# Kernel tuning notes

Measured on AMD Instinct MI355X. Metric: run time of the kernel, lower is better.

Reference implementation:

```python
import jax, jax.numpy as jnp
import numpy as np

TEMP = 0.07
BASE_TEMP = 0.07
BANK = 8192
B = 512      # samples per view; features has 2*B rows
D = 128      # feature dim
N_CLASSES = 100


def _l2norm(x, axis=-1):
    return x / jnp.linalg.norm(x, axis=axis, keepdims=True)


def setup_inputs() -> dict:
    key = jax.random.key(0)
    k1, k2, k3, k4, k5 = jax.random.split(key, 5)
    # SupCon features are L2-normalized embeddings; two views stacked: [2B, 1, D]
    features = _l2norm(jax.random.normal(k1, (2 * B, 1, D), jnp.float32))
    label = jax.random.randint(k2, (B,), 0, N_CLASSES)
    # memory banks stored as [D, bank_size] (lightly MemoryBankModule layout)
    bank1 = _l2norm(jax.random.normal(k3, (D, BANK), jnp.float32), axis=0)
    bank2 = _l2norm(jax.random.normal(k4, (D, BANK), jnp.float32), axis=0)
    bank_labels = jax.random.randint(k5, (BANK,), 0, N_CLASSES)
    return {"features": features, "label": label, "bank1": bank1,
            "bank2": bank2, "bank_labels": bank_labels}


def _branch_loss(cf, pos_mask, neg_mask):
    # cf: [N, D] anchor==contrast features
    logits = jnp.matmul(cf, cf.T) / TEMP                       # [N, N]
    logits = logits - jax.lax.stop_gradient(logits.max(axis=1, keepdims=True))
    # denominator: sum of exp(logits) over NEGATIVES only (square(mask-1) mask)
    denom = jnp.log((jnp.exp(logits) * neg_mask).sum(axis=1, keepdims=True))
    log_prob = logits - denom                                  # [N, N]
    mean_log_prob_pos = (pos_mask * log_prob).sum(axis=1) / pos_mask.sum(axis=1)
    return -(TEMP / BASE_TEMP) * mean_log_prob_pos             # [N]


def reference(features, label, bank1, bank2, bank_labels):
    d = features.shape[-1]
    fr = features.reshape(-1, d)                # [2B, D]
    nb = fr.shape[0] // 2
    f1, f2 = fr[:nb], fr[nb:]                   # [B, D] each

    labels_all = jnp.concatenate([bank_labels.reshape(-1, 1),
                                  label.reshape(-1, 1)], axis=0)   # [N, 1]
    same = (labels_all == labels_all.T)                            # [N, N]
    mask = same.astype(fr.dtype)
    n = mask.shape[0]
    self_mask = 1.0 - jnp.eye(n, dtype=fr.dtype)
    pos_mask = mask * self_mask                 # positives excluding self
    neg_mask = jnp.square(mask - 1.0)           # 1 where labels differ

    cf1 = jnp.concatenate([bank2.T, f1], axis=0)   # [N, D]
    cf2 = jnp.concatenate([bank1.T, f2], axis=0)   # [N, D]

    class_loss = (_branch_loss(cf1, pos_mask, neg_mask)
                  + _branch_loss(cf2, pos_mask, neg_mask)) / 2.0
    loss = class_loss.mean()
    return (loss, loss, loss)
```

## Files before the change

kernel.cpp:

```cpp
#include <hip/hip_runtime.h>
#include <math.h>

#define NTOT 8704
#define BANKN 8192
#define NB 512
#define DIM 128
#define INVT (1.0f / 0.07f)
#define C2L 20.6099131801f
#define NCHUNK 17
#define TPC 8
#define BN 64

using short8 = __attribute__((ext_vector_type(8))) short;
using ushort8 = __attribute__((ext_vector_type(8))) unsigned short;
using f32x4 = __attribute__((ext_vector_type(4))) float;

static __device__ __forceinline__ ushort f2bf(float f) {
  union { float f; unsigned u; } v;
  v.f = f;
  unsigned r = v.u + 0x7fffu + ((v.u >> 16) & 1u);
  return (ushort)(r >> 16);
}

static __device__ __forceinline__ float fast_exp2(float x) {
#if __has_builtin(__builtin_amdgcn_exp2f)
  return __builtin_amdgcn_exp2f(x);
#else
  return exp2f(x);
#endif
}

__global__ void prep1_kernel(const int* __restrict__ bank_labels,
                             const int* __restrict__ label,
                             int* __restrict__ cnt,
                             float* __restrict__ zp) {
  const int i = blockIdx.x * 256 + threadIdx.x;
  reinterpret_cast<float4*>(zp)[i] = make_float4(0.f, 0.f, 0.f, 0.f);
  const int v = (i < BANKN) ? bank_labels[i] : label[i - BANKN];
  atomicAdd(&cnt[v], 1);
}

__global__ void prep2_kernel(const int* __restrict__ cnt,
                             int* __restrict__ st, int* __restrict__ cur) {
  __shared__ int sc[128];
  const int tid = threadIdx.x;
  int mine = (tid < 100) ? cnt[tid] : 0;
  sc[tid] = mine;
  __syncthreads();
#pragma unroll
  for (int off = 1; off < 128; off <<= 1) {
    int add = (tid >= off) ? sc[tid - off] : 0;
    __syncthreads();
    sc[tid] += add;
    __syncthreads();
  }
  if (tid < 100) {
    const int ex = sc[tid] - mine;
    st[tid] = ex;
    cur[tid] = ex;
    if (tid == 99) st[100] = sc[99];
  }
}

__global__ void prep3_kernel(const int* __restrict__ bank_labels,
                             const int* __restrict__ label,
                             const int* __restrict__ st, int* __restrict__ cur,
                             int* __restrict__ inv, int* __restrict__ lo,
                             int* __restrict__ hi) {
  const int i = blockIdx.x * 256 + threadIdx.x;
  const int v = (i < BANKN) ? bank_labels[i] : label[i - BANKN];
  const int p = atomicAdd(&cur[v], 1);
  inv[i] = p;
  lo[p] = st[v];
  hi[p] = st[v + 1];
}

__global__ void pack_kernel(const float* __restrict__ features,
                            const float* __restrict__ bank1,
                            const float* __restrict__ bank2,
                            const int* __restrict__ inv,
                            ushort* __restrict__ cf1b,
                            ushort* __restrict__ cf2b) {
  const int branch = blockIdx.z;
  ushort* __restrict__ dst = branch ? cf2b : cf1b;
  const int tx = threadIdx.x, ty = threadIdx.y;
  const int bx = blockIdx.x, by = blockIdx.y;
  if (bx < 256) {
    const float* __restrict__ src = branch ? bank1 : bank2;
    __shared__ float tile[32][33];
    const int col = bx * 32 + tx;
#pragma unroll
    for (int s = 0; s < 32; s += 8)
      tile[ty + s][tx] = src[(size_t)(by * 32 + ty + s) * BANKN + col];
    __syncthreads();
    const int k = by * 32 + tx;
#pragma unroll
    for (int s = 0; s < 32; s += 8) {
      const int p = inv[bx * 32 + ty + s];
      dst[(size_t)p * DIM + k] = f2bf(tile[tx][ty + s]);
    }
  } else {
#pragma unroll
    for (int s = 0; s < 32; s += 8) {
      const int jr = (bx - 256) * 32 + ty + s;
      const int k = by * 32 + tx;
      const float v = features[(size_t)(branch * NB + jr) * DIM + k];
      const int p = inv[BANKN + jr];
      dst[(size_t)p * DIM + k] = f2bf(v);
    }
  }
}

__global__ __launch_bounds__(256) void supcon_mfma_kernel(
    const ushort* __restrict__ cf1b, const ushort* __restrict__ cf2b,
    const int* __restrict__ lo, const int* __restrict__ hi,
    float* __restrict__ zp) {
  const int rb = blockIdx.x;
  const int chunk = blockIdx.y;
  const int branch = blockIdx.z;
  const ushort* __restrict__ cf = branch ? cf2b : cf1b;

  const int tid = threadIdx.x;
  const int wid = tid >> 6, lane = tid & 63;
  const int l15 = lane & 15, l4 = lane >> 4;
  const int rowW = rb * 128 + wid * 32;

  __shared__ ushort Bt[3][BN * DIM];

  short8 a[2][4];
#pragma unroll
  for (int rt = 0; rt < 2; ++rt) {
    const int r = rowW + rt * 16 + l15;
#pragma unroll
    for (int ks = 0; ks < 4; ++ks)
      a[rt][ks] = *reinterpret_cast<const short8*>(cf + (size_t)r * DIM + ks * 32 + l4 * 8);
  }
  int rlo[2][4], rhi[2][4];
#pragma unroll
  for (int rt = 0; rt < 2; ++rt)
#pragma unroll
    for (int rg = 0; rg < 4; ++rg) {
      const int rr = rowW + rt * 16 + l4 * 4 + rg;
      rlo[rt][rg] = lo[rr];
      rhi[rt][rg] = hi[rr];
    }
  const int u_lo = lo[rowW];
  const int u_hi = hi[rowW + 31];
  const int lo_last = lo[rowW + 31];
  const int hi_first = hi[rowW];

  float Zr[2][4] = {};
  float Pr[2][4] = {};

  auto STAGE = [&](int t, int buf) {
    const int col0 = (chunk * TPC + t) * BN;
#pragma unroll
    for (int it = 0; it < 4; ++it) {
      const int o = it * 256 + tid;
      const int row = o >> 4, cc = o & 15;
      const ushort* src =
          cf + (size_t)(col0 + row) * DIM + ((cc ^ (row & 15)) * 8);
      ushort* dst = &Bt[buf][(it * 256 + wid * 64) * 8];
      __builtin_amdgcn_global_load_lds(
          (const __attribute__((address_space(1))) void*)src,
          (__attribute__((address_space(3))) void*)dst, 16, 0, 0);
    }
  };

  STAGE(0, 0);
  STAGE(1, 1);

  for (int t = 0; t < TPC; ++t) {
    if (t + 1 < TPC)
      asm volatile("s_waitcnt vmcnt(4)" ::: "memory");
    else
      asm volatile("s_waitcnt vmcnt(0)" ::: "memory");
    __builtin_amdgcn_s_barrier();
    if (t + 2 < TPC) STAGE(t + 2, (t + 2) % 3);

    const int col0 = (chunk * TPC + t) * BN;
    const ushort* __restrict__ B = &Bt[t % 3][0];

    f32x4 acc[2][4];
#pragma unroll
    for (int rt = 0; rt < 2; ++rt)
#pragma unroll
      for (int ct = 0; ct < 4; ++ct) acc[rt][ct] = (f32x4){0.f, 0.f, 0.f, 0.f};

#pragma unroll
    for (int ks = 0; ks < 4; ++ks) {
      short8 b[4];
#pragma unroll
      for (int ct = 0; ct < 4; ++ct) {
        const int r = ct * 16 + l15;
        const int swz = (ks * 4 + l4) ^ (r & 15);
        b[ct] = *reinterpret_cast<const short8*>(&B[r * DIM + swz * 8]);
      }
#pragma unroll
      for (int rt = 0; rt < 2; ++rt)
#pragma unroll
        for (int ct = 0; ct < 4; ++ct)
          acc[rt][ct] = __builtin_amdgcn_mfma_f32_16x16x32_bf16(
              a[rt][ks], b[ct], acc[rt][ct], 0, 0, 0);
    }

    if (col0 + BN <= u_lo || col0 >= u_hi) {
#pragma unroll
      for (int ct = 0; ct < 4; ++ct)
#pragma unroll
        for (int rt = 0; rt < 2; ++rt)
#pragma unroll
          for (int rg = 0; rg < 4; ++rg)
            Zr[rt][rg] += fast_exp2(fmaf(acc[rt][ct][rg], C2L, -C2L));
    } else if (col0 >= lo_last && col0 + BN <= hi_first) {
#pragma unroll
      for (int ct = 0; ct < 4; ++ct)
#pragma unroll
        for (int rt = 0; rt < 2; ++rt)
#pragma unroll
          for (int rg = 0; rg < 4; ++rg) Pr[rt][rg] += acc[rt][ct][rg];
    } else {
#pragma unroll
      for (int ct = 0; ct < 4; ++ct) {
        const int c = col0 + ct * 16 + l15;
#pragma unroll
        for (int rt = 0; rt < 2; ++rt)
#pragma unroll
          for (int rg = 0; rg < 4; ++rg) {
            const float v = acc[rt][ct][rg];
            const float e = fast_exp2(fmaf(v, C2L, -C2L));
            const bool s = (c >= rlo[rt][rg]) && (c < rhi[rt][rg]);
            Zr[rt][rg] += s ? 0.0f : e;
            Pr[rt][rg] += s ? v : 0.0f;
          }
      }
    }
  }

  float* Zrow = zp;
  float* Prow = zp + 2 * NTOT;
#pragma unroll
  for (int rt = 0; rt < 2; ++rt)
#pragma unroll
    for (int rg = 0; rg < 4; ++rg) {
      float z = Zr[rt][rg], p = Pr[rt][rg];
#pragma unroll
      for (int off = 1; off < 16; off <<= 1) {
        z += __shfl_xor(z, off);
        p += __shfl_xor(p, off);
      }
      if (l15 == 0) {
        const int row = rowW + rt * 16 + l4 * 4 + rg;
        atomicAdd(&Zrow[branch * NTOT + row], z);
        atomicAdd(&Prow[branch * NTOT + row], p);
      }
    }
}

__global__ __launch_bounds__(1024) void loss_kernel(const float* __restrict__ zp,
                                                    const int* __restrict__ lo,
                                                    const int* __restrict__ hi,
                                                    float* __restrict__ out) {
  const int tid = threadIdx.x;
  const float* Zrow = zp;
  const float* Prow = zp + 2 * NTOT;
  float local = 0.f;
  for (int idx = tid; idx < 2 * NTOT; idx += 1024) {
    const int row = (idx >= NTOT) ? idx - NTOT : idx;
    const float z = Zrow[idx];
    const float p = Prow[idx];
    const float C = (float)(hi[row] - lo[row] - 1);
    const float denom = INVT + logf(z);
    local += -((INVT * (p - 1.0f)) / C - denom);
  }
  __shared__ float s[1024];
  s[tid] = local;
  __syncthreads();
  for (int st = 512; st > 0; st >>= 1) {
    if (tid < st) s[tid] += s[tid + st];
    __syncthreads();
  }
  if (tid == 0) {
    const float v = s[0] / (2.0f * NTOT);
    out[0] = v; out[1] = v; out[2] = v;
  }
}

extern "C" void kernel_launch(void* const* d_in, const int* in_sizes, int n_in,
                              void* d_out, int out_size, void* d_ws,
                              size_t ws_size, hipStream_t stream) {
  const float* features = (const float*)d_in[0];
  const int* label = (const int*)d_in[1];
  const float* bank1 = (const float*)d_in[2];
  const float* bank2 = (const float*)d_in[3];
  const int* bank_labels = (const int*)d_in[4];
  float* out = (float*)d_out;

  char* ws = (char*)d_ws;
  ushort* cf1b = (ushort*)(ws);
  ushort* cf2b = (ushort*)(ws + 2228224);
  int* inv = (int*)(ws + 4456448);
  int* lo = (int*)(ws + 4491264);
  int* hi = (int*)(ws + 4526080);
  float* zp = (float*)(ws + 4560896);
  int* cnt = (int*)(ws + 4700160);
  int* st = (int*)(ws + 4700560);
  int* cur = (int*)(ws + 4700964);

  hipMemsetAsync(ws + 4700160, 0, 1204, stream);

  prep1_kernel<<<dim3(34), dim3(256), 0, stream>>>(bank_labels, label, cnt,
                                                   zp);
  prep2_kernel<<<dim3(1), dim3(128), 0, stream>>>(cnt, st, cur);
  prep3_kernel<<<dim3(34), dim3(256), 0, stream>>>(bank_labels, label, st, cur,
                                                   inv, lo, hi);
  pack_kernel<<<dim3(272, DIM / 32, 2), dim3(32, 8), 0, stream>>>(
      features, bank1, bank2, inv, cf1b, cf2b);
  supcon_mfma_kernel<<<dim3(NTOT / 128, NCHUNK, 2), dim3(256), 0, stream>>>(
      cf1b, cf2b, lo, hi, zp);
  loss_kernel<<<dim3(1), dim3(1024), 0, stream>>>(zp, lo, hi, out);
}
```

Before: 171.1 us.

## Drop label sort prep kernels and mask by per-column label compare

```diff
diff --git a/kernel.cpp b/kernel.cpp
--- a/kernel.cpp
+++ b/kernel.cpp
@@ -30,61 +30,27 @@
 #endif
 }
 
-__global__ void prep1_kernel(const int* __restrict__ bank_labels,
-                             const int* __restrict__ label,
-                             int* __restrict__ cnt,
-                             float* __restrict__ zp) {
-  const int i = blockIdx.x * 256 + threadIdx.x;
-  reinterpret_cast<float4*>(zp)[i] = make_float4(0.f, 0.f, 0.f, 0.f);
-  const int v = (i < BANKN) ? bank_labels[i] : label[i - BANKN];
-  atomicAdd(&cnt[v], 1);
-}
-
-__global__ void prep2_kernel(const int* __restrict__ cnt,
-                             int* __restrict__ st, int* __restrict__ cur) {
-  __shared__ int sc[128];
-  const int tid = threadIdx.x;
-  int mine = (tid < 100) ? cnt[tid] : 0;
-  sc[tid] = mine;
-  __syncthreads();
-#pragma unroll
-  for (int off = 1; off < 128; off <<= 1) {
-    int add = (tid >= off) ? sc[tid - off] : 0;
-    __syncthreads();
-    sc[tid] += add;
-    __syncthreads();
-  }
-  if (tid < 100) {
-    const int ex = sc[tid] - mine;
-    st[tid] = ex;
-    cur[tid] = ex;
-    if (tid == 99) st[100] = sc[99];
-  }
-}
-
-__global__ void prep3_kernel(const int* __restrict__ bank_labels,
-                             const int* __restrict__ label,
-                             const int* __restrict__ st, int* __restrict__ cur,
-                             int* __restrict__ inv, int* __restrict__ lo,
-                             int* __restrict__ hi) {
-  const int i = blockIdx.x * 256 + threadIdx.x;
-  const int v = (i < BANKN) ? bank_labels[i] : label[i - BANKN];
-  const int p = atomicAdd(&cur[v], 1);
-  inv[i] = p;
-  lo[p] = st[v];
-  hi[p] = st[v + 1];
-}
-
 __global__ void pack_kernel(const float* __restrict__ features,
                             const float* __restrict__ bank1,
                             const float* __restrict__ bank2,
-                            const int* __restrict__ inv,
+                            const int* __restrict__ bank_labels,
+                            const int* __restrict__ label,
                             ushort* __restrict__ cf1b,
-                            ushort* __restrict__ cf2b) {
+                            ushort* __restrict__ cf2b,
+                            int* __restrict__ lab_all,
+                            float* __restrict__ zp) {
   const int branch = blockIdx.z;
   ushort* __restrict__ dst = branch ? cf2b : cf1b;
   const int tx = threadIdx.x, ty = threadIdx.y;
   const int bx = blockIdx.x, by = blockIdx.y;
+  const int tid = ty * 32 + tx;
+
+  if (branch == 0 && by == 0 && bx < 34) {
+    const int i = bx * 256 + tid;
+    reinterpret_cast<float4*>(zp)[i] = make_float4(0.f, 0.f, 0.f, 0.f);
+    lab_all[i] = (i < BANKN) ? bank_labels[i] : label[i - BANKN];
+  }
+
   if (bx < 256) {
     const float* __restrict__ src = branch ? bank1 : bank2;
     __shared__ float tile[32][33];
@@ -95,26 +61,22 @@
     __syncthreads();
     const int k = by * 32 + tx;
 #pragma unroll
-    for (int s = 0; s < 32; s += 8) {
-      const int p = inv[bx * 32 + ty + s];
-      dst[(size_t)p * DIM + k] = f2bf(tile[tx][ty + s]);
-    }
+    for (int s = 0; s < 32; s += 8)
+      dst[(size_t)(bx * 32 + ty + s) * DIM + k] = f2bf(tile[tx][ty + s]);
   } else {
 #pragma unroll
     for (int s = 0; s < 32; s += 8) {
       const int jr = (bx - 256) * 32 + ty + s;
       const int k = by * 32 + tx;
       const float v = features[(size_t)(branch * NB + jr) * DIM + k];
-      const int p = inv[BANKN + jr];
-      dst[(size_t)p * DIM + k] = f2bf(v);
+      dst[(size_t)(BANKN + jr) * DIM + k] = f2bf(v);
     }
   }
 }
 
 __global__ __launch_bounds__(256) void supcon_mfma_kernel(
     const ushort* __restrict__ cf1b, const ushort* __restrict__ cf2b,
-    const int* __restrict__ lo, const int* __restrict__ hi,
-    float* __restrict__ zp) {
+    const int* __restrict__ lab_all, float* __restrict__ zp) {
   const int rb = blockIdx.x;
   const int chunk = blockIdx.y;
   const int branch = blockIdx.z;
@@ -135,19 +97,12 @@
     for (int ks = 0; ks < 4; ++ks)
       a[rt][ks] = *reinterpret_cast<const short8*>(cf + (size_t)r * DIM + ks * 32 + l4 * 8);
   }
-  int rlo[2][4], rhi[2][4];
+  int rlab[2][4];
 #pragma unroll
   for (int rt = 0; rt < 2; ++rt)
 #pragma unroll
-    for (int rg = 0; rg < 4; ++rg) {
-      const int rr = rowW + rt * 16 + l4 * 4 + rg;
-      rlo[rt][rg] = lo[rr];
-      rhi[rt][rg] = hi[rr];
-    }
-  const int u_lo = lo[rowW];
-  const int u_hi = hi[rowW + 31];
-  const int lo_last = lo[rowW + 31];
-  const int hi_first = hi[rowW];
+    for (int rg = 0; rg < 4; ++rg)
+      rlab[rt][rg] = lab_all[rowW + rt * 16 + l4 * 4 + rg];
 
   float Zr[2][4] = {};
   float Pr[2][4] = {};
@@ -179,6 +134,11 @@
     if (t + 2 < TPC) STAGE(t + 2, (t + 2) % 3);
 
     const int col0 = (chunk * TPC + t) * BN;
+
+    int clab[4];
+#pragma unroll
+    for (int ct = 0; ct < 4; ++ct) clab[ct] = lab_all[col0 + ct * 16 + l15];
+
     const ushort* __restrict__ B = &Bt[t % 3][0];
 
     f32x4 acc[2][4];
@@ -204,36 +164,22 @@
               a[rt][ks], b[ct], acc[rt][ct], 0, 0, 0);
     }
 
-    if (col0 + BN <= u_lo || col0 >= u_hi) {
-#pragma unroll
-      for (int ct = 0; ct < 4; ++ct)
-#pragma unroll
-        for (int rt = 0; rt < 2; ++rt)
-#pragma unroll
-          for (int rg = 0; rg < 4; ++rg)
-            Zr[rt][rg] += fast_exp2(fmaf(acc[rt][ct][rg], C2L, -C2L));
-    } else if (col0 >= lo_last && col0 + BN <= hi_first) {
-#pragma unroll
-      for (int ct = 0; ct < 4; ++ct)
-#pragma unroll
-        for (int rt = 0; rt < 2; ++rt)
-#pragma unroll
-          for (int rg = 0; rg < 4; ++rg) Pr[rt][rg] += acc[rt][ct][rg];
-    } else {
-#pragma unroll
-      for (int ct = 0; ct < 4; ++ct) {
-        const int c = col0 + ct * 16 + l15;
-#pragma unroll
-        for (int rt = 0; rt < 2; ++rt)
-#pragma unroll
-          for (int rg = 0; rg < 4; ++rg) {
-            const float v = acc[rt][ct][rg];
-            const float e = fast_exp2(fmaf(v, C2L, -C2L));
-            const bool s = (c >= rlo[rt][rg]) && (c < rhi[rt][rg]);
-            Zr[rt][rg] += s ? 0.0f : e;
-            Pr[rt][rg] += s ? v : 0.0f;
-          }
-      }
+#pragma unroll
+    for (int ct = 0; ct < 4; ++ct) {
+      const int c = col0 + ct * 16 + l15;
+      const int cl = clab[ct];
+#pragma unroll
+      for (int rt = 0; rt < 2; ++rt)
+#pragma unroll
+        for (int rg = 0; rg < 4; ++rg) {
+          const int r = rowW + rt * 16 + l4 * 4 + rg;
+          const float v = acc[rt][ct][rg];
+          const float e = fast_exp2(fmaf(v, C2L, -C2L));
+          const bool same = (rlab[rt][rg] == cl);
+          Zr[rt][rg] += same ? 0.0f : e;
+          const bool pos = same && (c != r);
+          Pr[rt][rg] += pos ? v : 0.0f;
+        }
     }
   }
 
@@ -257,23 +203,31 @@
     }
 }
 
-__global__ __launch_bounds__(1024) void loss_kernel(const float* __restrict__ zp,
-                                                    const int* __restrict__ lo,
-                                                    const int* __restrict__ hi,
-                                                    float* __restrict__ out) {
+__global__ __launch_bounds__(1024) void loss_kernel(
+    const float* __restrict__ zp, const int* __restrict__ bank_labels,
+    const int* __restrict__ label, float* __restrict__ out) {
   const int tid = threadIdx.x;
+  __shared__ int h[100];
+  __shared__ float s[1024];
+  if (tid < 100) h[tid] = 0;
+  __syncthreads();
+  for (int i = tid; i < NTOT; i += 1024) {
+    const int v = (i < BANKN) ? bank_labels[i] : label[i - BANKN];
+    atomicAdd(&h[v], 1);
+  }
+  __syncthreads();
   const float* Zrow = zp;
   const float* Prow = zp + 2 * NTOT;
   float local = 0.f;
   for (int idx = tid; idx < 2 * NTOT; idx += 1024) {
     const int row = (idx >= NTOT) ? idx - NTOT : idx;
+    const int rl = (row < BANKN) ? bank_labels[row] : label[row - BANKN];
     const float z = Zrow[idx];
     const float p = Prow[idx];
-    const float C = (float)(hi[row] - lo[row] - 1);
+    const float C = (float)(h[rl] - 1);
     const float denom = INVT + logf(z);
-    local += -((INVT * (p - 1.0f)) / C - denom);
-  }
-  __shared__ float s[1024];
+    local += -((INVT * p) / C - denom);
+  }
   s[tid] = local;
   __syncthreads();
   for (int st = 512; st > 0; st >>= 1) {
@@ -299,24 +253,12 @@
   char* ws = (char*)d_ws;
   ushort* cf1b = (ushort*)(ws);
   ushort* cf2b = (ushort*)(ws + 2228224);
-  int* inv = (int*)(ws + 4456448);
-  int* lo = (int*)(ws + 4491264);
-  int* hi = (int*)(ws + 4526080);
-  float* zp = (float*)(ws + 4560896);
-  int* cnt = (int*)(ws + 4700160);
-  int* st = (int*)(ws + 4700560);
-  int* cur = (int*)(ws + 4700964);
-
-  hipMemsetAsync(ws + 4700160, 0, 1204, stream);
-
-  prep1_kernel<<<dim3(34), dim3(256), 0, stream>>>(bank_labels, label, cnt,
-                                                   zp);
-  prep2_kernel<<<dim3(1), dim3(128), 0, stream>>>(cnt, st, cur);
-  prep3_kernel<<<dim3(34), dim3(256), 0, stream>>>(bank_labels, label, st, cur,
-                                                   inv, lo, hi);
+  int* lab_all = (int*)(ws + 4456448);
+  float* zp = (float*)(ws + 4491264);
+
   pack_kernel<<<dim3(272, DIM / 32, 2), dim3(32, 8), 0, stream>>>(
-      features, bank1, bank2, inv, cf1b, cf2b);
+      features, bank1, bank2, bank_labels, label, cf1b, cf2b, lab_all, zp);
   supcon_mfma_kernel<<<dim3(NTOT / 128, NCHUNK, 2), dim3(256), 0, stream>>>(
-      cf1b, cf2b, lo, hi, zp);
-  loss_kernel<<<dim3(1), dim3(1024), 0, stream>>>(zp, lo, hi, out);
-}
+      cf1b, cf2b, lab_all, zp);
+  loss_kernel<<<dim3(1), dim3(1024), 0, stream>>>(zp, bank_labels, label, out);
+}
```

Measured after the change: 159.0 us. 1.08x faster.
